# Kernel optimization log

Measured on AMD Instinct MI355X. Metric: run time of the kernel, lower is better.

## Reference

```python
import jax, jax.numpy as jnp
import numpy as np

H = 16  # n_heads


def _ln(x, g, b, eps=1e-5):
    m = x.mean(-1, keepdims=True)
    v = ((x - m) ** 2).mean(-1, keepdims=True)
    return (x - m) / jnp.sqrt(v + eps) * g + b


def setup_inputs() -> dict:
    key = jax.random.key(0)
    ks = jax.random.split(key, 10)
    b, lq, d, dff, L = 2, 1024, 1024, 4096, 4
    s = 0.02
    return {
        "x": jax.random.normal(ks[0], (b, lq, d), jnp.float32),
        "memory_bank": jax.random.normal(ks[1], (L, b, lq, d), jnp.float32),
        "attn_mask": jax.random.bernoulli(ks[2], 0.3, (b, lq, lq)),
        "ln1_g": jnp.ones((d,), jnp.float32),
        "ln1_b": jnp.zeros((d,), jnp.float32),
        "Wq": jax.random.normal(ks[3], (d, d), jnp.float32) * s,
        "Wk": jax.random.normal(ks[4], (d, d), jnp.float32) * s,
        "Wv": jax.random.normal(ks[5], (d, d), jnp.float32) * s,
        "Wo": jax.random.normal(ks[6], (d, d), jnp.float32) * s,
        "ln2_g": jnp.ones((d,), jnp.float32),
        "ln2_b": jnp.zeros((d,), jnp.float32),
        "W1": jax.random.normal(ks[7], (d, dff), jnp.float32) * s,
        "b1": jnp.zeros((dff,), jnp.float32),
        "W2": jax.random.normal(ks[8], (dff, d), jnp.float32) * s,
        "b2": jnp.zeros((d,), jnp.float32),
    }


def reference(x, memory_bank, attn_mask, ln1_g, ln1_b, Wq, Wk, Wv, Wo,
              ln2_g, ln2_b, W1, b1, W2, b2):
    # x: [b, lq, d]; memory_bank: [L, b, lk, d]; attn_mask: [b, lq, lk] bool (True = masked)
    b, lq, d = x.shape
    dh = d // H
    # preprocess_attn: LayerNorm (eval mode -> dropouts are identity)
    q = _ln(x, ln1_g, ln1_b)
    # grow memory bank with current normalized input
    mem = jnp.concatenate([memory_bank, q[None]], axis=0)  # [L+1, b, lk, d]
    L, _, lk, _ = mem.shape
    # projections (bias-free); key/value projected per layer then flattened over (L, lk)
    pq = (q @ Wq).reshape(b, lq, H, dh).transpose(0, 2, 1, 3) * (dh ** -0.5)  # [b,h,lq,dh]
    pk = (mem @ Wk).transpose(1, 0, 2, 3).reshape(b, L * lk, H, dh).transpose(0, 2, 1, 3)
    pv = (mem @ Wv).transpose(1, 0, 2, 3).reshape(b, L * lk, H, dh).transpose(0, 2, 1, 3)
    scores = jnp.einsum('bhqd,bhkd->bhqk', pq, pk)           # [b,h,lq,L*lk]
    scores = scores.reshape(b, H, lq, L, lk)
    scores = jnp.where(attn_mask[:, None, :, None, :], -jnp.inf, scores)
    attn = jax.nn.softmax(scores.reshape(b, H, lq, L * lk), axis=-1)
    ctx = jnp.einsum('bhqk,bhkd->bhqd', attn, pv)            # [b,h,lq,dh]
    ctx = ctx.transpose(0, 2, 1, 3).reshape(b, lq, d)
    attn_out = ctx @ Wo
    # postprocess_attn: residual add
    x2 = x + attn_out
    # FFN: LayerNorm -> Linear -> ReLU -> Linear -> residual
    f = _ln(x2, ln2_g, ln2_b)
    f = jax.nn.relu(f @ W1 + b1) @ W2 + b2
    out = x2 + f
    return (out, mem)
```

## Files before the change

kernel.cpp:

```cpp
#include <hip/hip_runtime.h>
#include <hip/hip_bf16.h>

typedef __attribute__((ext_vector_type(8))) __bf16 bf16x8;
typedef __attribute__((ext_vector_type(4))) __bf16 bf16x4;
typedef __attribute__((ext_vector_type(4))) float f32x4;
typedef __attribute__((ext_vector_type(16))) float f32x16;

#define MFMA16(a, b, c) __builtin_amdgcn_mfma_f32_16x16x32_bf16((a), (b), (c), 0, 0, 0)
#define MFMA32(a, b, c) __builtin_amdgcn_mfma_f32_32x32x16_bf16((a), (b), (c), 0, 0, 0)
#define LOG2E 1.4426950408889634f

static __device__ __forceinline__ float exp2_fast(float x) {
    float r; asm("v_exp_f32 %0, %1" : "=v"(r) : "v"(x)); return r;
}

__device__ __forceinline__ void gll16(const void* g, void* l) {
    __builtin_amdgcn_global_load_lds((const __attribute__((address_space(1))) void*)g,
                                     (__attribute__((address_space(3))) void*)l,
                                     16, 0, 0);
}

__global__ __launch_bounds__(256) void prep_kernel(const float* __restrict__ bank,
                                                   float* __restrict__ mem_out,
                                                   __bf16* __restrict__ membf,
                                                   const float* __restrict__ x,
                                                   const float* __restrict__ g,
                                                   const float* __restrict__ bta,
                                                   float* __restrict__ q_out,
                                                   __bf16* __restrict__ qbf,
                                                   const float* __restrict__ Wq,
                                                   const float* __restrict__ Wk,
                                                   const float* __restrict__ Wv,
                                                   __bf16* __restrict__ Wq_t,
                                                   __bf16* __restrict__ Wkv_t,
                                                   const unsigned char* __restrict__ mask,
                                                   unsigned int* __restrict__ mbits) {
    __shared__ float rs[4], rs2[4];
    __shared__ float tile[32][33];
    int blk = blockIdx.x;
    if (blk < 2048) {
        int i = blk * 256 + threadIdx.x;
        const float4* i4 = (const float4*)bank;
        float4* o4 = (float4*)mem_out;
        for (; i < 2097152; i += 2048 * 256) {
            float4 v = i4[i];
            o4[i] = v;
            if (membf) {
                bf16x4 ob = {(__bf16)v.x, (__bf16)v.y, (__bf16)v.z, (__bf16)v.w};
                ((bf16x4*)membf)[i] = ob;
            }
        }
    } else if (blk < 4096) {
        int row = blk - 2048;
        const float4 v = ((const float4*)(x + (size_t)row * 1024))[threadIdx.x];
        float s = v.x + v.y + v.z + v.w;
        float s2 = v.x * v.x + v.y * v.y + v.z * v.z + v.w * v.w;
#pragma unroll
        for (int off = 1; off < 64; off <<= 1) {
            s += __shfl_xor(s, off);
            s2 += __shfl_xor(s2, off);
        }
        int wv = threadIdx.x >> 6;
        if ((threadIdx.x & 63) == 0) { rs[wv] = s; rs2[wv] = s2; }
        __syncthreads();
        s = rs[0] + rs[1] + rs[2] + rs[3];
        s2 = rs2[0] + rs2[1] + rs2[2] + rs2[3];
        float mean = s * (1.0f / 1024.0f);
        float var = s2 * (1.0f / 1024.0f) - mean * mean;
        float rstd = rsqrtf(var + 1e-5f);
        float4 gg = ((const float4*)g)[threadIdx.x];
        float4 bb = ((const float4*)bta)[threadIdx.x];
        float4 o;
        o.x = (v.x - mean) * rstd * gg.x + bb.x;
        o.y = (v.y - mean) * rstd * gg.y + bb.y;
        o.z = (v.z - mean) * rstd * gg.z + bb.z;
        o.w = (v.w - mean) * rstd * gg.w + bb.w;
        ((float4*)(q_out + (size_t)row * 1024))[threadIdx.x] = o;
        if (qbf) {
            bf16x4 ob = {(__bf16)o.x, (__bf16)o.y, (__bf16)o.z, (__bf16)o.w};
            ((bf16x4*)(qbf + (size_t)row * 1024))[threadIdx.x] = ob;
        }
    } else if (blk < 7168) {
        int w = blk - 4096;
        int sel = w >> 10, within = w & 1023;
        const float* in = (sel == 0) ? Wq : ((sel == 1) ? Wk : Wv);
        __bf16* out = (sel == 0) ? Wq_t : (Wkv_t + (size_t)(sel - 1) * 1048576);
        int k0 = (within >> 5) * 32, n0 = (within & 31) * 32;
        int tx = threadIdx.x & 31, ty = threadIdx.x >> 5;
#pragma unroll
        for (int i = 0; i < 4; i++)
            tile[ty + i * 8][tx] = in[(size_t)(k0 + ty + i * 8) * 1024 + n0 + tx];
        __syncthreads();
#pragma unroll
        for (int i = 0; i < 4; i++)
            out[(size_t)(n0 + ty + i * 8) * 1024 + k0 + tx] = (__bf16)tile[tx][ty + i * 8];
    } else if (mbits) {
        int row = blk - 7168;
        const unsigned char* mrow = mask + (size_t)row * 1024;
        int wv = threadIdx.x >> 6, l = threadIdx.x & 63;
        unsigned long long* dst = (unsigned long long*)(mbits + (size_t)row * 32);
#pragma unroll
        for (int i = 0; i < 4; i++) {
            int key = i * 256 + wv * 64 + l;
            unsigned long long bal = __ballot(mrow[key] != 0);
            if (l == 0) dst[i * 4 + wv] = bal;
        }
    }
}

__global__ __launch_bounds__(256) void vtr_kernel(const __bf16* __restrict__ PV,
                                                  __bf16* __restrict__ PVt) {
    __shared__ __bf16 tile[64][72];
    int w = blockIdx.x;
    int bh = w / 80, kt = w % 80;
    int b = bh >> 4, h = bh & 15;
    int lidx = kt >> 4, i0 = (kt & 15) * 64;
    int kg0 = lidx * 2048 + b * 1024 + i0;
    int r = threadIdx.x >> 2, c16 = (threadIdx.x & 3) * 16;
    const __bf16* src = PV + (size_t)(kg0 + r) * 1024 + h * 64 + c16;
    *(bf16x8*)&tile[r][c16] = *(const bf16x8*)src;
    *(bf16x8*)&tile[r][c16 + 8] = *(const bf16x8*)(src + 8);
    __syncthreads();
    int dh = threadIdx.x >> 2, k0 = (threadIdx.x & 3) * 16;
    bf16x8 o0, o1;
#pragma unroll
    for (int j = 0; j < 8; j++) {
        o0[j] = tile[k0 + j][dh];
        o1[j] = tile[k0 + 8 + j][dh];
    }
    __bf16* dst = PVt + (size_t)(bh * 64 + dh) * 5120 + kt * 64 + k0;
    *(bf16x8*)dst = o0;
    *(bf16x8*)(dst + 8) = o1;
}

__global__ __launch_bounds__(256) void ln_kernel(const float* __restrict__ x,
                                                 const float* __restrict__ g,
                                                 const float* __restrict__ bta,
                                                 __bf16* __restrict__ outb) {
    int row = blockIdx.x;
    const float4 v = ((const float4*)(x + (size_t)row * 1024))[threadIdx.x];
    float s = v.x + v.y + v.z + v.w;
    float s2 = v.x * v.x + v.y * v.y + v.z * v.z + v.w * v.w;
#pragma unroll
    for (int off = 1; off < 64; off <<= 1) {
        s += __shfl_xor(s, off);
        s2 += __shfl_xor(s2, off);
    }
    __shared__ float rs[4], rs2[4];
    int wv = threadIdx.x >> 6;
    if ((threadIdx.x & 63) == 0) { rs[wv] = s; rs2[wv] = s2; }
    __syncthreads();
    s = rs[0] + rs[1] + rs[2] + rs[3];
    s2 = rs2[0] + rs2[1] + rs2[2] + rs2[3];
    float mean = s * (1.0f / 1024.0f);
    float var = s2 * (1.0f / 1024.0f) - mean * mean;
    float rstd = rsqrtf(var + 1e-5f);
    float4 gg = ((const float4*)g)[threadIdx.x];
    float4 bb = ((const float4*)bta)[threadIdx.x];
    bf16x4 ob;
    ob[0] = (__bf16)((v.x - mean) * rstd * gg.x + bb.x);
    ob[1] = (__bf16)((v.y - mean) * rstd * gg.y + bb.y);
    ob[2] = (__bf16)((v.z - mean) * rstd * gg.z + bb.z);
    ob[3] = (__bf16)((v.w - mean) * rstd * gg.w + bb.w);
    ((bf16x4*)(outb + (size_t)row * 1024))[threadIdx.x] = ob;
}

__global__ __launch_bounds__(256) void comb_ln2(const float* __restrict__ pc0,
                                                const float* __restrict__ pc1,
                                                const float* __restrict__ x,
                                                const float* __restrict__ g,
                                                const float* __restrict__ bta,
                                                float* __restrict__ x2,
                                                __bf16* __restrict__ fln) {
    int row = blockIdx.x;
    int idx = row * 256 + threadIdx.x;
    float4 a = ((const float4*)pc0)[idx];
    float4 b = ((const float4*)pc1)[idx];
    float4 r = ((const float4*)x)[idx];
    float4 v;
    v.x = a.x + b.x + r.x;
    v.y = a.y + b.y + r.y;
    v.z = a.z + b.z + r.z;
    v.w = a.w + b.w + r.w;
    ((float4*)x2)[idx] = v;
    float s = v.x + v.y + v.z + v.w;
    float s2 = v.x * v.x + v.y * v.y + v.z * v.z + v.w * v.w;
#pragma unroll
    for (int off = 1; off < 64; off <<= 1) {
        s += __shfl_xor(s, off);
        s2 += __shfl_xor(s2, off);
    }
    __shared__ float rs[4], rs2[4];
    int wv = threadIdx.x >> 6;
    if ((threadIdx.x & 63) == 0) { rs[wv] = s; rs2[wv] = s2; }
    __syncthreads();
    s = rs[0] + rs[1] + rs[2] + rs[3];
    s2 = rs2[0] + rs2[1] + rs2[2] + rs2[3];
    float mean = s * (1.0f / 1024.0f);
    float var = s2 * (1.0f / 1024.0f) - mean * mean;
    float rstd = rsqrtf(var + 1e-5f);
    float4 gg = ((const float4*)g)[threadIdx.x];
    float4 bb = ((const float4*)bta)[threadIdx.x];
    bf16x4 ob;
    ob[0] = (__bf16)((v.x - mean) * rstd * gg.x + bb.x);
    ob[1] = (__bf16)((v.y - mean) * rstd * gg.y + bb.y);
    ob[2] = (__bf16)((v.z - mean) * rstd * gg.z + bb.z);
    ob[3] = (__bf16)((v.w - mean) * rstd * gg.w + bb.w);
    ((bf16x4*)(fln + (size_t)row * 1024))[threadIdx.x] = ob;
}

__device__ __forceinline__ void tr_body(const float* __restrict__ in, __bf16* __restrict__ out,
                                        int K, int N, int k0, int n0) {
    __shared__ float tile[32][33];
    int tx = threadIdx.x & 31, ty = threadIdx.x >> 5;
#pragma unroll
    for (int i = 0; i < 4; i++)
        tile[ty + i * 8][tx] = in[(size_t)(k0 + ty + i * 8) * N + n0 + tx];
    __syncthreads();
#pragma unroll
    for (int i = 0; i < 4; i++)
        out[(size_t)(n0 + ty + i * 8) * K + k0 + tx] = (__bf16)tile[tx][ty + i * 8];
}

__global__ __launch_bounds__(256) void tr_late(const float* __restrict__ Wo,
                                               const float* __restrict__ W1,
                                               const float* __restrict__ W2,
                                               __bf16* __restrict__ Wo_t,
                                               __bf16* __restrict__ W1_t,
                                               __bf16* __restrict__ W2_t) {
    int w = blockIdx.x;
    const float* in;
    __bf16* out;
    int K, N, k0, n0;
    if (w < 1024) {
        in = Wo; out = Wo_t; K = 1024; N = 1024; n0 = (w & 31) * 32; k0 = (w >> 5) * 32;
    } else if (w < 5120) {
        int v = w - 1024;
        in = W1; out = W1_t; K = 1024; N = 4096; n0 = (v & 127) * 32; k0 = (v >> 7) * 32;
    } else {
        int v = w - 5120;
        in = W2; out = W2_t; K = 4096; N = 1024; n0 = (v & 31) * 32; k0 = (v >> 5) * 32;
    }
    tr_body(in, out, K, N, k0, n0);
}

template <int EPI, bool ABF16>
__device__ __forceinline__ void gemm_core(const void* __restrict__ Av,
                                          const __bf16* __restrict__ Bt,
                                          void* __restrict__ Cout,
                                          const float* __restrict__ bias,
                                          const float* __restrict__ res,
                                          int N, int lda, int ldb, int klen,
                                          float scale, int bm, int bn) {
    constexpr int LDA = ABF16 ? 32 : 40;
    __shared__ __bf16 As[128 * LDA];
    __shared__ __bf16 Bs[128 * 32];

    int t = threadIdx.x;
    int lane = t & 63, wave = t >> 6;
    int wm = (wave >> 1) * 64, wn = (wave & 1) * 64;
    int l16 = lane & 15, l4 = lane >> 4;

    f32x4 acc[4][4];
#pragma unroll
    for (int m = 0; m < 4; m++)
#pragma unroll
        for (int n = 0; n < 4; n++) acc[m][n] = (f32x4){0.f, 0.f, 0.f, 0.f};

    int srow = t >> 2;
    int scol = (t & 3) * 8;
    int ar = t >> 1, ak = (t & 1) * 16;
    const __bf16* Ab = (const __bf16*)Av;
    const float* Af = (const float*)Av;

    for (int k0 = 0; k0 < klen; k0 += 32) {
        gll16(Bt + (size_t)(bn + srow) * ldb + (k0 + scol), &Bs[wave * 512]);
        gll16(Bt + (size_t)(bn + 64 + srow) * ldb + (k0 + scol), &Bs[2048 + wave * 512]);
        if constexpr (ABF16) {
            gll16(Ab + (size_t)(bm + srow) * lda + (k0 + scol), &As[wave * 512]);
            gll16(Ab + (size_t)(bm + 64 + srow) * lda + (k0 + scol), &As[2048 + wave * 512]);
        } else {
            const float* ap = Af + (size_t)(bm + ar) * lda + k0 + ak;
            float4 f0 = ((const float4*)ap)[0];
            float4 f1 = ((const float4*)ap)[1];
            float4 f2 = ((const float4*)ap)[2];
            float4 f3 = ((const float4*)ap)[3];
            float ta[16] = {f0.x, f0.y, f0.z, f0.w, f1.x, f1.y, f1.z, f1.w,
                            f2.x, f2.y, f2.z, f2.w, f3.x, f3.y, f3.z, f3.w};
            bf16x8 v0, v1;
#pragma unroll
            for (int j = 0; j < 8; j++) { v0[j] = (__bf16)ta[j]; v1[j] = (__bf16)ta[j + 8]; }
            *(bf16x8*)&As[ar * 40 + ak] = v0;
            *(bf16x8*)&As[ar * 40 + ak + 8] = v1;
        }
        __syncthreads();

        bf16x8 af[4], bfr[4];
#pragma unroll
        for (int m = 0; m < 4; m++) af[m] = *(const bf16x8*)&As[(wm + m * 16 + l16) * LDA + l4 * 8];
#pragma unroll
        for (int n = 0; n < 4; n++) bfr[n] = *(const bf16x8*)&Bs[(wn + n * 16 + l16) * 32 + l4 * 8];
#pragma unroll
        for (int m = 0; m < 4; m++)
#pragma unroll
            for (int n = 0; n < 4; n++) acc[m][n] = MFMA16(af[m], bfr[n], acc[m][n]);
        __syncthreads();
    }

#pragma unroll
    for (int m = 0; m < 4; m++) {
#pragma unroll
        for (int r = 0; r < 4; r++) {
            int row = bm + wm + m * 16 + l4 * 4 + r;
#pragma unroll
            for (int n = 0; n < 4; n++) {
                int col = bn + wn + n * 16 + l16;
                float c = acc[m][n][r];
                size_t idx = (size_t)row * N + col;
                if (EPI == 0) {
                    ((__bf16*)Cout)[idx] = (__bf16)(c * scale);
                } else if (EPI == 1) {
                    ((float*)Cout)[idx] = c + res[idx];
                } else if (EPI == 2) {
                    ((__bf16*)Cout)[idx] = (__bf16)fmaxf(c + bias[col], 0.0f);
                } else if (EPI == 3) {
                    ((float*)Cout)[idx] = c + bias[col] + res[idx];
                } else {
                    ((float*)Cout)[idx] = c;
                }
            }
        }
    }
}

template <int EPI, bool ABF16>
__global__ __launch_bounds__(256) void gemm_bt(const void* __restrict__ Av,
                                               const __bf16* __restrict__ Bt,
                                               void* __restrict__ Cout,
                                               const float* __restrict__ bias,
                                               const float* __restrict__ res,
                                               int N, int K, float scale, int nbx) {
    int q = gridDim.x >> 3;
    int swz = (blockIdx.x & 7) * q + (blockIdx.x >> 3);
    int bn = (swz % nbx) * 128;
    int bm = (swz / nbx) * 128;
    gemm_core<EPI, ABF16>(Av, Bt, Cout, bias, res, N, K, K, K, scale, bm, bn);
}

template <bool ABF16>
__global__ __launch_bounds__(256) void gemm_proj(const void* __restrict__ Akv,
                                                 const __bf16* __restrict__ Wkv_t,
                                                 __bf16* __restrict__ PK,
                                                 __bf16* __restrict__ PV,
                                                 const void* __restrict__ Aq,
                                                 const __bf16* __restrict__ Wq_t,
                                                 __bf16* __restrict__ Pq) {
    int q = gridDim.x >> 3;
    int swz = (blockIdx.x & 7) * q + (blockIdx.x >> 3);
    if (swz < 1280) {
        int bn = (swz & 15) * 128, bm = (swz >> 4) * 128;
        __bf16* C = (bn < 1024) ? PK : PV;
        int bnl = bn & 1023;
        const __bf16* Bt = Wkv_t + ((size_t)(bn & 1024) << 10);
        gemm_core<0, ABF16>(Akv, Bt, C, nullptr, nullptr, 1024, 1024, 1024, 1024, 1.0f, bm, bnl);
    } else {
        int p = swz - 1280;
        int bn = (p & 7) * 128, bm = (p >> 3) * 128;
        gemm_core<0, ABF16>(Aq, Wq_t, Pq, nullptr, nullptr, 1024, 1024, 1024, 1024,
                            0.125f * LOG2E, bm, bn);
    }
}

__global__ __launch_bounds__(256) void gemm_w2(const __bf16* __restrict__ h1,
                                               const __bf16* __restrict__ W2_t,
                                               float* __restrict__ pc0,
                                               float* __restrict__ pc1) {
    int q = gridDim.x >> 3;
    int swz = (blockIdx.x & 7) * q + (blockIdx.x >> 3);
    int half = swz >> 7;
    int p = swz & 127;
    int bn = (p & 7) * 128, bm = (p >> 3) * 128;
    int koff = half * 2048;
    gemm_core<4, true>(h1 + koff, W2_t + koff, half ? pc1 : pc0, nullptr, nullptr,
                       1024, 4096, 4096, 2048, 1.0f, bm, bn);
}

__global__ __launch_bounds__(256) void gemm_wo(const __bf16* __restrict__ ctx,
                                               const __bf16* __restrict__ Wo_t,
                                               float* __restrict__ pc0,
                                               float* __restrict__ pc1) {
    int q = gridDim.x >> 3;
    int swz = (blockIdx.x & 7) * q + (blockIdx.x >> 3);
    int half = swz >> 7;
    int p = swz & 127;
    int bn = (p & 7) * 128, bm = (p >> 3) * 128;
    int koff = half * 512;
    gemm_core<4, true>(ctx + koff, Wo_t + koff, half ? pc1 : pc0, nullptr, nullptr,
                       1024, 1024, 1024, 512, 1.0f, bm, bn);
}

__global__ __launch_bounds__(256) void comb_kernel(const float* __restrict__ pc0,
                                                   const float* __restrict__ pc1,
                                                   const float* __restrict__ bias,
                                                   const float* __restrict__ res,
                                                   float* __restrict__ out) {
    int i = blockIdx.x * 256 + threadIdx.x;
    float4 a = ((const float4*)pc0)[i];
    float4 b = ((const float4*)pc1)[i];
    float4 r = ((const float4*)res)[i];
    float4 o;
    o.x = a.x + b.x + r.x;
    o.y = a.y + b.y + r.y;
    o.z = a.z + b.z + r.z;
    o.w = a.w + b.w + r.w;
    if (bias) {
        float4 bb = ((const float4*)bias)[i & 255];
        o.x += bb.x; o.y += bb.y; o.z += bb.z; o.w += bb.w;
    }
    ((float4*)out)[i] = o;
}

__device__ __forceinline__ void softmax_p(const f32x16& s0, const f32x16& s1,
                                          unsigned int mka, unsigned int mkb,
                                          int hi, float& lsum, bf16x8* pf) {
    unsigned int ow[8][2];
#pragma unroll
    for (int g = 0; g < 4; g++) {
        bf16x4 p0, p1;
#pragma unroll
        for (int m = 0; m < 4; m++) {
            float e = exp2_fast(s0[g * 4 + m]);
            e = ((mka >> (g * 8 + hi * 4 + m)) & 1u) ? 0.0f : e;
            lsum += e;
            p0[m] = (__bf16)e;
            float e2 = exp2_fast(s1[g * 4 + m]);
            e2 = ((mkb >> (g * 8 + hi * 4 + m)) & 1u) ? 0.0f : e2;
            lsum += e2;
            p1[m] = (__bf16)e2;
        }
        ow[g][0] = ((unsigned int*)&p0)[0];
        ow[g][1] = ((unsigned int*)&p0)[1];
        ow[4 + g][0] = ((unsigned int*)&p1)[0];
        ow[4 + g][1] = ((unsigned int*)&p1)[1];
    }
#pragma unroll
    for (int ks = 0; ks < 4; ks++) {
        unsigned int a0 = ow[2 * ks][0], b0 = ow[2 * ks + 1][0];
        unsigned int a1 = ow[2 * ks][1], b1 = ow[2 * ks + 1][1];
        asm volatile("v_permlane32_swap_b32 %0, %1" : "+v"(a0), "+v"(b0));
        asm volatile("v_permlane32_swap_b32 %0, %1" : "+v"(a1), "+v"(b1));
        unsigned int* pp = (unsigned int*)&pf[ks];
        pp[0] = a0; pp[1] = a1; pp[2] = b0; pp[3] = b1;
    }
}

#define NCHP 20
__global__ __launch_bounds__(256, 2) void attn_part(const __bf16* __restrict__ Pq,
                                                    const __bf16* __restrict__ PK,
                                                    const __bf16* __restrict__ PVt,
                                                    const unsigned int* __restrict__ mbits,
                                                    __bf16* __restrict__ pacc,
                                                    float* __restrict__ pl) {
    int bh = blockIdx.x;
    int b = bh >> 4, h = bh & 15;
    int rng = blockIdx.z;
    int wave = threadIdx.x >> 6, lane = threadIdx.x & 63;
    int l32 = lane & 31, hi = lane >> 5;
    int q0 = blockIdx.y * 256 + wave * 64;

    __shared__ __bf16 KB[2][64][64];
    __shared__ __bf16 VB[2][64][64];

    bf16x8 qf[2][4];
#pragma unroll
    for (int tile = 0; tile < 2; tile++) {
        const __bf16* pqrow = Pq + (size_t)(b * 1024 + q0 + tile * 32 + l32) * 1024 + h * 64 + hi * 8;
#pragma unroll
        for (int ds = 0; ds < 4; ds++) qf[tile][ds] = *(const bf16x8*)(pqrow + ds * 16);
    }

    f32x16 acc00, acc01, acc10, acc11;
#pragma unroll
    for (int i = 0; i < 16; i++) { acc00[i] = 0.f; acc01[i] = 0.f; acc10[i] = 0.f; acc11[i] = 0.f; }
    float lsum0 = 0.0f, lsum1 = 0.0f;

    const unsigned int* mrow0 = mbits + (size_t)(b * 1024 + q0 + l32) * 32;
    const unsigned int* mrow1 = mbits + (size_t)(b * 1024 + q0 + 32 + l32) * 32;

    int kgbase = rng * 1280;

    int idxA = wave * 8 + (lane >> 3);
    int idxB = (wave + 4) * 8 + (lane >> 3);
    int GA = (idxA ^ (idxA >> 3)) & 7;
    int GB = (idxB ^ (idxB >> 3)) & 7;
    int swA = (((lane & 7) ^ GA) << 4);
    int swB = (((lane & 7) ^ GB) << 4);
    size_t koffA = (size_t)idxA * 2048 + swA;
    size_t koffB = (size_t)idxB * 2048 + swB;
    size_t voffA = (size_t)idxA * 10240 + swA;
    size_t voffB = (size_t)idxB * 10240 + swB;

    int kmod = kgbase & 1023;
    const char* pkc = (const char*)PK + ((size_t)((kgbase >> 10) * 2048 + b * 1024 + kmod)) * 2048
                      + (size_t)h * 128;
    const char* pvc = (const char*)PVt + (size_t)(bh * 64) * 10240 + (size_t)kgbase * 2;

#define STAGE(BUF)                                            \
    do {                                                      \
        gll16(pkc + koffA, &KB[BUF][wave * 8][0]);            \
        gll16(pkc + koffB, &KB[BUF][(wave + 4) * 8][0]);      \
        gll16(pvc + voffA, &VB[BUF][wave * 8][0]);            \
        gll16(pvc + voffB, &VB[BUF][(wave + 4) * 8][0]);      \
    } while (0)
#define ADV()                                                          \
    do {                                                               \
        int st = (kmod + 64 >= 1024) ? (64 + 1024) : 64;               \
        kmod = (kmod + 64) & 1023;                                     \
        pkc += (size_t)st * 2048;                                      \
        pvc += 128;                                                    \
    } while (0)

    STAGE(0);
    ADV();
    int kd0 = (kgbase & 1023) >> 5;
    unsigned int mk0a = mrow0[kd0], mk0b = mrow0[kd0 + 1];
    unsigned int mk1a = mrow1[kd0], mk1b = mrow1[kd0 + 1];

    int Gr0 = (l32 ^ (l32 >> 3)) & 7;
    int r1v = 32 + l32;
    int Gr1 = (r1v ^ (r1v >> 3)) & 7;

    for (int t = 0; t < NCHP; t++) {
        int buf = t & 1;
        __syncthreads();
        if (t + 1 < NCHP) {
            STAGE(buf ^ 1);
            ADV();
        }
        unsigned int nk0a = 0, nk0b = 0, nk1a = 0, nk1b = 0;
        if (t + 1 < NCHP) {
            int kdn = ((kgbase + (t + 1) * 64) & 1023) >> 5;
            nk0a = mrow0[kdn]; nk0b = mrow0[kdn + 1];
            nk1a = mrow1[kdn]; nk1b = mrow1[kdn + 1];
        }

        const __bf16* KsF = &KB[buf][0][0];
        const __bf16* VtF = &VB[buf][0][0];

        f32x16 s00, s01, s10, s11;
#pragma unroll
        for (int i = 0; i < 16; i++) { s00[i] = 0.f; s01[i] = 0.f; s10[i] = 0.f; s11[i] = 0.f; }
        __builtin_amdgcn_s_setprio(1);
#pragma unroll
        for (int ds = 0; ds < 4; ds++) {
            bf16x8 ka0 = *(const bf16x8*)&KsF[l32 * 64 + (((ds * 2 + hi) ^ Gr0) << 3)];
            bf16x8 ka1 = *(const bf16x8*)&KsF[r1v * 64 + (((ds * 2 + hi) ^ Gr1) << 3)];
            s00 = MFMA32(ka0, qf[0][ds], s00);
            s10 = MFMA32(ka0, qf[1][ds], s10);
            s01 = MFMA32(ka1, qf[0][ds], s01);
            s11 = MFMA32(ka1, qf[1][ds], s11);
        }
        __builtin_amdgcn_s_setprio(0);

        bf16x8 pf0[4], pf1[4];
        softmax_p(s00, s01, mk0a, mk0b, hi, lsum0, pf0);
        softmax_p(s10, s11, mk1a, mk1b, hi, lsum1, pf1);

        mk0a = nk0a; mk0b = nk0b; mk1a = nk1a; mk1b = nk1b;

        __builtin_amdgcn_s_setprio(1);
#pragma unroll
        for (int ks = 0; ks < 4; ks++) {
            bf16x8 vf0 = *(const bf16x8*)&VtF[l32 * 64 + (((ks * 2 + hi) ^ Gr0) << 3)];
            bf16x8 vf1 = *(const bf16x8*)&VtF[r1v * 64 + (((ks * 2 + hi) ^ Gr1) << 3)];
            acc00 = MFMA32(vf0, pf0[ks], acc00);
            acc01 = MFMA32(vf1, pf0[ks], acc01);
            acc10 = MFMA32(vf0, pf1[ks], acc10);
            acc11 = MFMA32(vf1, pf1[ks], acc11);
        }
        __builtin_amdgcn_s_setprio(0);
    }
#undef STAGE
#undef ADV

    lsum0 += __shfl_xor(lsum0, 32);
    lsum1 += __shfl_xor(lsum1, 32);

    size_t blk = ((size_t)(bh * 4 + blockIdx.y) * 4 + rng);
    __bf16* pa0 = pacc + blk * 16384 + (size_t)(wave * 64 + l32) * 64;
    __bf16* pa1 = pacc + blk * 16384 + (size_t)(wave * 64 + 32 + l32) * 64;
#pragma unroll
    for (int g = 0; g < 4; g++) {
        bf16x4 o00, o01, o10, o11;
#pragma unroll
        for (int m = 0; m < 4; m++) {
            o00[m] = (__bf16)acc00[g * 4 + m];
            o01[m] = (__bf16)acc01[g * 4 + m];
            o10[m] = (__bf16)acc10[g * 4 + m];
            o11[m] = (__bf16)acc11[g * 4 + m];
        }
        *(bf16x4*)&pa0[g * 8 + hi * 4] = o00;
        *(bf16x4*)&pa0[32 + g * 8 + hi * 4] = o01;
        *(bf16x4*)&pa1[g * 8 + hi * 4] = o10;
        *(bf16x4*)&pa1[32 + g * 8 + hi * 4] = o11;
    }
    if (hi == 0) {
        pl[blk * 256 + wave * 64 + l32] = lsum0;
        pl[blk * 256 + wave * 64 + 32 + l32] = lsum1;
    }
}

__global__ __launch_bounds__(512) void attn_comb(const __bf16* __restrict__ pacc,
                                                 const float* __restrict__ pl,
                                                 __bf16* __restrict__ ctx) {
    int bh = blockIdx.x, qb = blockIdx.y;
    int b = bh >> 4, h = bh & 15;
    int q = threadIdx.x >> 1, dhalf = (threadIdx.x & 1) * 32;
    float acc[32];
#pragma unroll
    for (int j = 0; j < 32; j++) acc[j] = 0.0f;
    float l = 0.0f;
    size_t blk0 = ((size_t)(bh * 4 + qb)) * 4;
#pragma unroll
    for (int rng = 0; rng < 4; rng++) {
        size_t base = (blk0 + rng) * 16384 + (size_t)q * 64 + dhalf;
#pragma unroll
        for (int v = 0; v < 4; v++) {
            bf16x8 a = *(const bf16x8*)&pacc[base + v * 8];
#pragma unroll
            for (int j = 0; j < 8; j++) acc[v * 8 + j] += (float)a[j];
        }
        l += pl[(blk0 + rng) * 256 + q];
    }
    float inv = 1.0f / l;
    __bf16* crow = ctx + ((size_t)(b * 1024 + qb * 256 + q) << 10) + h * 64 + dhalf;
#pragma unroll
    for (int v = 0; v < 4; v++) {
        bf16x8 o;
#pragma unroll
        for (int j = 0; j < 8; j++) o[j] = (__bf16)(acc[v * 8 + j] * inv);
        *(bf16x8*)&crow[v * 8] = o;
    }
}

#define KHALF 2560
#define CK 64
#define NCH 40
__global__ __launch_bounds__(512, 4) void attn_kernel(const __bf16* __restrict__ Pq,
                                                      const __bf16* __restrict__ PK,
                                                      const __bf16* __restrict__ PV,
                                                      const unsigned char* __restrict__ mask,
                                                      __bf16* __restrict__ ctx) {
    int bh = blockIdx.x;
    int b = bh >> 4, h = bh & 15;
    int wave = threadIdx.x >> 6, lane = threadIdx.x & 63;
    int grp = wave >> 2, wv = wave & 3;
    int l16 = lane & 15, l4 = lane >> 4;
    int q0 = blockIdx.y * 64 + wv * 16;

    __shared__ __bf16 Ks[2][64][72];
    __shared__ __bf16 Vt[2][64][72];
    __shared__ __bf16 Ps[8][16][72];

    const f32x4 fzero = {0.f, 0.f, 0.f, 0.f};

    bf16x8 qf[2];
    {
        const __bf16* pqrow = Pq + (size_t)(b * 1024 + q0 + l16) * 1024 + h * 64;
        qf[0] = *(const bf16x8*)(pqrow + l4 * 8);
        qf[1] = *(const bf16x8*)(pqrow + 32 + l4 * 8);
    }

    f32x4 accT[4];
#pragma unroll
    for (int n = 0; n < 4; n++) accT[n] = fzero;
    float lsum = 0.0f;

    const unsigned char* mrow_p = mask + (size_t)b * (1024u * 1024u) + (size_t)(q0 + l16) * 1024;

    int tl = threadIdx.x & 255;
    int skey = tl >> 2;
    int sd0 = (tl & 3) << 4;
    int kgbase = grp * KHALF;

    bf16x8 rk0, rk1, rv0, rv1;
    unsigned int mk[4], mkn[4];
    {
        int kg = kgbase + skey;
        int lidx = kg >> 10, i = kg & 1023;
        size_t off = (size_t)(lidx * 2048 + b * 1024 + i) * 1024 + h * 64 + sd0;
        rk0 = *(const bf16x8*)(PK + off);
        rk1 = *(const bf16x8*)(PK + off + 8);
        rv0 = *(const bf16x8*)(PV + off);
        rv1 = *(const bf16x8*)(PV + off + 8);
        int kloc = kgbase & 1023;
#pragma unroll
        for (int tile = 0; tile < 4; tile++)
            mk[tile] = *(const unsigned int*)(mrow_p + kloc + tile * 16 + l4 * 4);
    }

    for (int t = 0; t < NCH; t++) {
        *(bf16x8*)&Ks[grp][skey][sd0] = rk0;
        *(bf16x8*)&Ks[grp][skey][sd0 + 8] = rk1;
#pragma unroll
        for (int j = 0; j < 8; j++) {
            int row = sd0 + j;
            Vt[grp][row][skey ^ ((row >> 3) << 3)] = rv0[j];
            int row2 = sd0 + 8 + j;
            Vt[grp][row2][skey ^ ((row2 >> 3) << 3)] = rv1[j];
        }
        __syncthreads();

        if (t + 1 < NCH) {
            int kg = kgbase + (t + 1) * CK + skey;
            int lidx = kg >> 10, i = kg & 1023;
            size_t off = (size_t)(lidx * 2048 + b * 1024 + i) * 1024 + h * 64 + sd0;
            rk0 = *(const bf16x8*)(PK + off);
            rk1 = *(const bf16x8*)(PK + off + 8);
            rv0 = *(const bf16x8*)(PV + off);
            rv1 = *(const bf16x8*)(PV + off + 8);
            int kloc = (kgbase + (t + 1) * CK) & 1023;
#pragma unroll
            for (int tile = 0; tile < 4; tile++)
                mkn[tile] = *(const unsigned int*)(mrow_p + kloc + tile * 16 + l4 * 4);
        }

        f32x4 s[4];
        __builtin_amdgcn_s_setprio(1);
#pragma unroll
        for (int tile = 0; tile < 4; tile++) {
            bf16x8 ka = *(const bf16x8*)&Ks[grp][tile * 16 + l16][l4 * 8];
            bf16x8 kb = *(const bf16x8*)&Ks[grp][tile * 16 + l16][32 + l4 * 8];
            f32x4 sz = fzero;
            sz = MFMA16(ka, qf[0], sz);
            sz = MFMA16(kb, qf[1], sz);
            s[tile] = sz;
        }
        __builtin_amdgcn_s_setprio(0);

        float psum = 0.0f;
#pragma unroll
        for (int tile = 0; tile < 4; tile++) {
            bf16x4 pk_;
#pragma unroll
            for (int r = 0; r < 4; r++) {
                float e = exp2_fast(s[tile][r]);
                e = ((mk[tile] >> (r * 8)) & 255u) ? 0.0f : e;
                psum += e;
                pk_[r] = (__bf16)e;
            }
            *(bf16x4*)&Ps[wave][l16][tile * 16 + l4 * 4] = pk_;
        }
        lsum += psum;
#pragma unroll
        for (int tile = 0; tile < 4; tile++) mk[tile] = mkn[tile];

        __builtin_amdgcn_s_setprio(1);
#pragma unroll
        for (int kk = 0; kk < 2; kk++) {
            bf16x8 pf = *(const bf16x8*)&Ps[wave][l16][kk * 32 + l4 * 8];
#pragma unroll
            for (int n = 0; n < 4; n++) {
                int row = n * 16 + l16;
                int colblk = (kk * 32 + l4 * 8) ^ ((row >> 3) << 3);
                bf16x8 vf = *(const bf16x8*)&Vt[grp][row][colblk];
                accT[n] = MFMA16(vf, pf, accT[n]);
            }
        }
        __builtin_amdgcn_s_setprio(0);
        __syncthreads();
    }

    lsum += __shfl_xor(lsum, 16);
    lsum += __shfl_xor(lsum, 32);

    float* exAcc = (float*)&Ks[0][0][0];
    float* exL = (float*)&Vt[0][0][0];
    if (grp == 1) {
#pragma unroll
        for (int n = 0; n < 4; n++)
            *(f32x4*)&exAcc[(wv * 16 + l16) * 68 + n * 16 + l4 * 4] = accT[n];
        if (l4 == 0) exL[wv * 16 + l16] = lsum;
    }
    __syncthreads();
    if (grp == 0) {
        int qi = wv * 16 + l16;
        float inv = 1.0f / (lsum + exL[qi]);
        __bf16* crow = ctx + ((size_t)(b * 1024 + q0 + l16) << 10) + h * 64;
#pragma unroll
        for (int n = 0; n < 4; n++) {
            f32x4 a1 = *(const f32x4*)&exAcc[qi * 68 + n * 16 + l4 * 4];
            bf16x4 o;
#pragma unroll
            for (int r = 0; r < 4; r++) o[r] = (__bf16)((accT[n][r] + a1[r]) * inv);
            *(bf16x4*)&crow[n * 16 + l4 * 4] = o;
        }
    }
}

extern "C" void kernel_launch(void* const* d_in, const int* in_sizes, int n_in,
                              void* d_out, int out_size, void* d_ws, size_t ws_size,
                              hipStream_t stream) {
    const float* x = (const float*)d_in[0];
    const float* memory_bank = (const float*)d_in[1];
    const unsigned char* attn_mask = (const unsigned char*)d_in[2];
    const float* ln1_g = (const float*)d_in[3];
    const float* ln1_b = (const float*)d_in[4];
    const float* Wq = (const float*)d_in[5];
    const float* Wk = (const float*)d_in[6];
    const float* Wv = (const float*)d_in[7];
    const float* Wo = (const float*)d_in[8];
    const float* ln2_g = (const float*)d_in[9];
    const float* ln2_b = (const float*)d_in[10];
    const float* W1 = (const float*)d_in[11];
    const float* b1 = (const float*)d_in[12];
    const float* W2 = (const float*)d_in[13];
    const float* b2 = (const float*)d_in[14];

    float* out = (float*)d_out;
    float* mem_out = out + 2097152;
    float* q_out = mem_out + 4 * 2097152;

    char* ws = (char*)d_ws;
    bool big = ws_size >= (71ull << 20);

    __bf16* PK = (__bf16*)ws;
    __bf16* PV = (__bf16*)(ws + (20ull << 20));
    __bf16 *Pq, *Wq_t, *Wkv_t, *ctx, *membf = nullptr, *qbf = nullptr;
    __bf16* PVt = nullptr;
    __bf16* pacc = nullptr;
    float* plv = nullptr;
    unsigned int* mbits = nullptr;
    if (big) {
        membf = (__bf16*)(ws + (40ull << 20));
        qbf = membf + (size_t)8192 * 1024;
        Wq_t = (__bf16*)(ws + (60ull << 20));
        Wkv_t = (__bf16*)(ws + (62ull << 20));
        Pq = (__bf16*)(ws + (66ull << 20));
        mbits = (unsigned int*)(ws + (70ull << 20));
        PVt = (__bf16*)(ws + (40ull << 20));
        pacc = (__bf16*)(ws + (20ull << 20));
        plv = (float*)(ws + (36ull << 20));
        ctx = (__bf16*)(ws + (60ull << 20));
    } else {
        Pq = (__bf16*)(ws + (40ull << 20));
        Wq_t = (__bf16*)(ws + (44ull << 20));
        Wkv_t = (__bf16*)(ws + (46ull << 20));
        ctx = (__bf16*)(ws + (44ull << 20));
    }
    __bf16* Wo_t = (__bf16*)ws;
    __bf16* W1_t = (__bf16*)(ws + (2ull << 20));
    __bf16* W2_t = (__bf16*)(ws + (10ull << 20));
    float* x2 = (float*)(ws + (18ull << 20));
    __bf16* fln = (__bf16*)(ws + (26ull << 20));
    __bf16* h1 = (__bf16*)(ws + (30ull << 20));
    float* wo_pc0 = (float*)(ws + (30ull << 20));
    float* wo_pc1 = (float*)(ws + (38ull << 20));
    float* pc0 = (float*)(ws + (46ull << 20));
    float* pc1 = (float*)(ws + (54ull << 20));

    prep_kernel<<<big ? 9216 : 7168, 256, 0, stream>>>(memory_bank, mem_out, membf, x,
                                                       ln1_g, ln1_b, q_out, qbf,
                                                       Wq, Wk, Wv, Wq_t, Wkv_t,
                                                       attn_mask, mbits);

    if (big)
        gemm_proj<true><<<1408, 256, 0, stream>>>(membf, Wkv_t, PK, PV, qbf, Wq_t, Pq);
    else
        gemm_proj<false><<<1408, 256, 0, stream>>>(mem_out, Wkv_t, PK, PV, q_out, Wq_t, Pq);

    if (big) {
        vtr_kernel<<<2560, 256, 0, stream>>>(PV, PVt);
        attn_part<<<dim3(32, 4, 4), 256, 0, stream>>>(Pq, PK, PVt, mbits, pacc, plv);
        attn_comb<<<dim3(32, 4), 512, 0, stream>>>(pacc, plv, ctx);
    } else {
        attn_kernel<<<dim3(32, 16), 512, 0, stream>>>(Pq, PK, PV, attn_mask, ctx);
    }

    tr_late<<<9216, 256, 0, stream>>>(Wo, W1, W2, Wo_t, W1_t, W2_t);

    if (big) {
        gemm_wo<<<256, 256, 0, stream>>>(ctx, Wo_t, wo_pc0, wo_pc1);
        comb_ln2<<<2048, 256, 0, stream>>>(wo_pc0, wo_pc1, x, ln2_g, ln2_b, x2, fln);
    } else {
        gemm_bt<1, true><<<128, 256, 0, stream>>>(ctx, Wo_t, x2, nullptr, x, 1024, 1024, 1.0f, 8);
        ln_kernel<<<2048, 256, 0, stream>>>(x2, ln2_g, ln2_b, fln);
    }
    gemm_bt<2, true><<<512, 256, 0, stream>>>(fln, W1_t, h1, b1, nullptr, 4096, 1024, 1.0f, 32);
    if (big) {
        gemm_w2<<<256, 256, 0, stream>>>(h1, W2_t, pc0, pc1);
        comb_kernel<<<2048, 256, 0, stream>>>(pc0, pc1, b2, x2, out);
    } else {
        gemm_bt<3, true><<<128, 256, 0, stream>>>(h1, W2_t, out, b2, x2, 1024, 4096, 1.0f, 8);
    }
}
```

Baseline: 272.8 us.

## Fuse weight transposes into attention kernel to overlap with attention tail

Merges the late weight transpose/convert kernel into the attention partial kernel as extra blocks in a single 1D grid, so transpose work can fill CUs while attention blocks run. The transposed weight buffers are relocated to a dedicated workspace region so they no longer alias attention scratch, which raises the workspace threshold for the fast path. This removes one kernel launch and the idle tail; the trade-off is shared memory sized for the attention blocks and possible contention between the two workloads.

Result: faster. 267.1 us (-2.1%).

```diff
diff --git a/kernel.cpp b/kernel.cpp
--- a/kernel.cpp
+++ b/kernel.cpp
@@ -455,21 +455,56 @@
 }
 
 #define NCHP 20
-__global__ __launch_bounds__(256, 2) void attn_part(const __bf16* __restrict__ Pq,
-                                                    const __bf16* __restrict__ PK,
-                                                    const __bf16* __restrict__ PVt,
-                                                    const unsigned int* __restrict__ mbits,
-                                                    __bf16* __restrict__ pacc,
-                                                    float* __restrict__ pl) {
-    int bh = blockIdx.x;
+__global__ __launch_bounds__(256, 2) void attn_tr(const __bf16* __restrict__ Pq,
+                                                  const __bf16* __restrict__ PK,
+                                                  const __bf16* __restrict__ PVt,
+                                                  const unsigned int* __restrict__ mbits,
+                                                  __bf16* __restrict__ pacc,
+                                                  float* __restrict__ pl,
+                                                  const float* __restrict__ Wo,
+                                                  const float* __restrict__ W1,
+                                                  const float* __restrict__ W2,
+                                                  __bf16* __restrict__ Wo_t,
+                                                  __bf16* __restrict__ W1_t,
+                                                  __bf16* __restrict__ W2_t) {
+    __shared__ char smem[32768];
+    int blk = blockIdx.x;
+    if (blk >= 512) {
+        float (*tile)[33] = (float(*)[33])smem;
+        int w = blk - 512;
+        const float* in;
+        __bf16* out;
+        int K, N, k0, n0;
+        if (w < 1024) {
+            in = Wo; out = Wo_t; K = 1024; N = 1024; n0 = (w & 31) * 32; k0 = (w >> 5) * 32;
+        } else if (w < 5120) {
+            int v = w - 1024;
+            in = W1; out = W1_t; K = 1024; N = 4096; n0 = (v & 127) * 32; k0 = (v >> 7) * 32;
+        } else {
+            int v = w - 5120;
+            in = W2; out = W2_t; K = 4096; N = 1024; n0 = (v & 31) * 32; k0 = (v >> 5) * 32;
+        }
+        int tx = threadIdx.x & 31, ty = threadIdx.x >> 5;
+#pragma unroll
+        for (int i = 0; i < 4; i++)
+            tile[ty + i * 8][tx] = in[(size_t)(k0 + ty + i * 8) * N + n0 + tx];
+        __syncthreads();
+#pragma unroll
+        for (int i = 0; i < 4; i++)
+            out[(size_t)(n0 + ty + i * 8) * K + k0 + tx] = (__bf16)tile[tx][ty + i * 8];
+        return;
+    }
+
+    __bf16 (*KB)[64][64] = (__bf16(*)[64][64])smem;
+    __bf16 (*VB)[64][64] = (__bf16(*)[64][64])(smem + 16384);
+
+    int bh = blk & 31;
+    int qb = (blk >> 5) & 3;
+    int rng = blk >> 7;
     int b = bh >> 4, h = bh & 15;
-    int rng = blockIdx.z;
     int wave = threadIdx.x >> 6, lane = threadIdx.x & 63;
     int l32 = lane & 31, hi = lane >> 5;
-    int q0 = blockIdx.y * 256 + wave * 64;
-
-    __shared__ __bf16 KB[2][64][64];
-    __shared__ __bf16 VB[2][64][64];
+    int q0 = qb * 256 + wave * 64;
 
     bf16x8 qf[2][4];
 #pragma unroll
@@ -586,9 +621,9 @@
     lsum0 += __shfl_xor(lsum0, 32);
     lsum1 += __shfl_xor(lsum1, 32);
 
-    size_t blk = ((size_t)(bh * 4 + blockIdx.y) * 4 + rng);
-    __bf16* pa0 = pacc + blk * 16384 + (size_t)(wave * 64 + l32) * 64;
-    __bf16* pa1 = pacc + blk * 16384 + (size_t)(wave * 64 + 32 + l32) * 64;
+    size_t oblk = ((size_t)(bh * 4 + qb) * 4 + rng);
+    __bf16* pa0 = pacc + oblk * 16384 + (size_t)(wave * 64 + l32) * 64;
+    __bf16* pa1 = pacc + oblk * 16384 + (size_t)(wave * 64 + 32 + l32) * 64;
 #pragma unroll
     for (int g = 0; g < 4; g++) {
         bf16x4 o00, o01, o10, o11;
@@ -605,8 +640,8 @@
         *(bf16x4*)&pa1[32 + g * 8 + hi * 4] = o11;
     }
     if (hi == 0) {
-        pl[blk * 256 + wave * 64 + l32] = lsum0;
-        pl[blk * 256 + wave * 64 + 32 + l32] = lsum1;
+        pl[oblk * 256 + wave * 64 + l32] = lsum0;
+        pl[oblk * 256 + wave * 64 + 32 + l32] = lsum1;
     }
 }
 
@@ -822,11 +857,12 @@
     float* q_out = mem_out + 4 * 2097152;
 
     char* ws = (char*)d_ws;
-    bool big = ws_size >= (71ull << 20);
+    bool big = ws_size >= (89ull << 20);
 
     __bf16* PK = (__bf16*)ws;
     __bf16* PV = (__bf16*)(ws + (20ull << 20));
     __bf16 *Pq, *Wq_t, *Wkv_t, *ctx, *membf = nullptr, *qbf = nullptr;
+    __bf16 *Wo_t, *W1_t, *W2_t;
     __bf16* PVt = nullptr;
     __bf16* pacc = nullptr;
     float* plv = nullptr;
@@ -838,6 +874,9 @@
         Wkv_t = (__bf16*)(ws + (62ull << 20));
         Pq = (__bf16*)(ws + (66ull << 20));
         mbits = (unsigned int*)(ws + (70ull << 20));
+        Wo_t = (__bf16*)(ws + (71ull << 20));
+        W1_t = (__bf16*)(ws + (73ull << 20));
+        W2_t = (__bf16*)(ws + (81ull << 20));
         PVt = (__bf16*)(ws + (40ull << 20));
         pacc = (__bf16*)(ws + (20ull << 20));
         plv = (float*)(ws + (36ull << 20));
@@ -847,10 +886,10 @@
         Wq_t = (__bf16*)(ws + (44ull << 20));
         Wkv_t = (__bf16*)(ws + (46ull << 20));
         ctx = (__bf16*)(ws + (44ull << 20));
-    }
-    __bf16* Wo_t = (__bf16*)ws;
-    __bf16* W1_t = (__bf16*)(ws + (2ull << 20));
-    __bf16* W2_t = (__bf16*)(ws + (10ull << 20));
+        Wo_t = (__bf16*)ws;
+        W1_t = (__bf16*)(ws + (2ull << 20));
+        W2_t = (__bf16*)(ws + (10ull << 20));
+    }
     float* x2 = (float*)(ws + (18ull << 20));
     __bf16* fln = (__bf16*)(ws + (26ull << 20));
     __bf16* h1 = (__bf16*)(ws + (30ull << 20));
@@ -871,13 +910,13 @@
 
     if (big) {
         vtr_kernel<<<2560, 256, 0, stream>>>(PV, PVt);
-        attn_part<<<dim3(32, 4, 4), 256, 0, stream>>>(Pq, PK, PVt, mbits, pacc, plv);
+        attn_tr<<<9728, 256, 0, stream>>>(Pq, PK, PVt, mbits, pacc, plv,
+                                          Wo, W1, W2, Wo_t, W1_t, W2_t);
         attn_comb<<<dim3(32, 4), 512, 0, stream>>>(pacc, plv, ctx);
     } else {
         attn_kernel<<<dim3(32, 16), 512, 0, stream>>>(Pq, PK, PV, attn_mask, ctx);
-    }
-
-    tr_late<<<9216, 256, 0, stream>>>(Wo, W1, W2, Wo_t, W1_t, W2_t);
+        tr_late<<<9216, 256, 0, stream>>>(Wo, W1, W2, Wo_t, W1_t, W2_t);
+    }
 
     if (big) {
         gemm_wo<<<256, 256, 0, stream>>>(ctx, Wo_t, wo_pc0, wo_pc1);
```
